# Kernel optimization log

Hardware: AMD Instinct MI355X
Metric: run time of the kernel (lower is better)

Reference implementation:

```python
import jax, jax.numpy as jnp
import numpy as np

N_LABELS = 16
LABEL_DIM = 128
BN_EPS = 1e-5


def setup_inputs() -> dict:
    key = jax.random.key(0)
    k1, k2 = jax.random.split(key, 2)
    B, T, D = 8, 512, 768
    return {
        "features": jax.random.normal(k1, (B, T, D), dtype=jnp.float32),
        "mask": jnp.ones((B, T), dtype=bool),
        "bn_gamma": jnp.ones((D,), dtype=jnp.float32),
        "bn_beta": jnp.zeros((D,), dtype=jnp.float32),
        "ff_w": jax.random.normal(k2, (LABEL_DIM * N_LABELS * 2, D), dtype=jnp.float32) * 0.02,
        "ff_b": jnp.zeros((LABEL_DIM * N_LABELS * 2,), dtype=jnp.float32),
        "label_bias": jnp.zeros((N_LABELS,), dtype=jnp.float32),
    }


def reference(features, mask, bn_gamma, bn_beta, ff_w, ff_b, label_bias):
    B, T, D = features.shape
    m = mask.astype(features.dtype)[..., None]  # [B,T,1]
    denom = jnp.maximum(m.sum(), 1.0)
    # FlatBatchNorm (training mode): stats over masked tokens, zeros elsewhere
    mean = (features * m).sum(axis=(0, 1)) / denom
    var = (((features - mean) ** 2) * m).sum(axis=(0, 1)) / denom
    normed = (features - mean) * jax.lax.rsqrt(var + BN_EPS) * bn_gamma + bn_beta
    feats = normed * m  # res[mask]=flat, zeros elsewhere
    # FFN + relu -> [B,T,n_labels,label_dim,2]
    h = jax.nn.relu(jnp.einsum('btd,od->bto', feats, ff_w) + ff_b)
    h = h.reshape(B, T, N_LABELS, LABEL_DIM, 2)
    start_f = h[..., 0]  # [B,T,L,D]
    end_f = h[..., 1]
    # biaffine span scores: [B, L, T_start, T_end]
    scores = jnp.einsum('bsld,beld->blse', start_f, end_f) + label_bias[None, :, None, None]
    triu = jnp.triu(jnp.ones((T, T), dtype=bool))
    spans_mask = triu[None, None] & mask[:, None, :, None] & mask[:, None, None, :]  # [B,L,T,T] via broadcast
    spans_mask = jnp.broadcast_to(spans_mask, scores.shape)
    return scores, spans_mask
```

## Files before the change

kernel.cpp:

```cpp
#include <hip/hip_runtime.h>

#define B_    8
#define T_    512
#define D_    768
#define L_    16
#define DL_   128
#define M_    4096
#define BN_EPS 1e-5f

typedef __attribute__((ext_vector_type(8))) short short8;
typedef __attribute__((ext_vector_type(4))) float f32x4;

__device__ inline unsigned short f2bf(float x) {
    unsigned int u = __float_as_uint(x);
    return (unsigned short)((u + 0x7fffu + ((u >> 16) & 1u)) >> 16);
}

__device__ inline void async16(const unsigned short* gptr, unsigned short* lptr) {
    __builtin_amdgcn_global_load_lds(
        (const __attribute__((address_space(1))) void*)gptr,
        (__attribute__((address_space(3))) void*)lptr, 16, 0, 0);
}

__global__ void k_stats(const float* __restrict__ f, const int* __restrict__ mask,
                        float* __restrict__ stats) {
    int tid = threadIdx.x;
    int t0  = blockIdx.x * 16;
    float s0 = 0.f, s1 = 0.f, s2 = 0.f, q0 = 0.f, q1 = 0.f, q2 = 0.f;
    for (int tt = 0; tt < 16; ++tt) {
        int t = t0 + tt;
        float m = mask[t] ? 1.f : 0.f;
        const float* row = f + (size_t)t * D_;
        float x0 = row[tid];
        float x1 = row[tid + 256];
        float x2 = row[tid + 512];
        s0 += x0 * m; q0 += x0 * x0 * m;
        s1 += x1 * m; q1 += x1 * x1 * m;
        s2 += x2 * m; q2 += x2 * x2 * m;
    }
    atomicAdd(&stats[tid      ], s0);
    atomicAdd(&stats[tid + 256], s1);
    atomicAdd(&stats[tid + 512], s2);
    atomicAdd(&stats[768 + tid      ], q0);
    atomicAdd(&stats[768 + tid + 256], q1);
    atomicAdd(&stats[768 + tid + 512], q2);
    if (tid == 0) {
        int c = 0;
        for (int tt = 0; tt < 16; ++tt) c += (mask[t0 + tt] ? 1 : 0);
        atomicAdd(&stats[1536], (float)c);
    }
}

__global__ void k_finalize(const float* __restrict__ gamma, const float* __restrict__ beta,
                           float* __restrict__ stats) {
    int d = threadIdx.x;
    float denom = fmaxf(stats[1536], 1.f);
    float mean  = stats[d] / denom;
    float var   = fmaxf(stats[768 + d] / denom - mean * mean, 0.f);
    float sc    = gamma[d] * rsqrtf(var + BN_EPS);
    stats[2048 + d] = sc;
    stats[2816 + d] = beta[d] - mean * sc;
}

__global__ void k_prep(const float4* __restrict__ f4, const int* __restrict__ mask,
                       const float* __restrict__ stats, unsigned short* __restrict__ feats,
                       const float4* __restrict__ w4, unsigned short* __restrict__ wbf) {
    int bx = blockIdx.x;
    if (bx < 3072) {
        int i  = bx * 256 + threadIdx.x;
        int d4 = i % (D_ / 4);
        int t  = i / (D_ / 4);
        float m = mask[t] ? 1.f : 0.f;
        float4 v = f4[i];
        int d = d4 * 4;
        ushort4 o;
        o.x = f2bf((v.x * stats[2048 + d + 0] + stats[2816 + d + 0]) * m);
        o.y = f2bf((v.y * stats[2048 + d + 1] + stats[2816 + d + 1]) * m);
        o.z = f2bf((v.z * stats[2048 + d + 2] + stats[2816 + d + 2]) * m);
        o.w = f2bf((v.w * stats[2048 + d + 3] + stats[2816 + d + 3]) * m);
        ((ushort4*)feats)[i] = o;
    } else {
        int i  = (bx - 3072) * 256 + threadIdx.x;
        int o  = i / 192, cg = i % 192;
        int nr = (o & 1) * 2048 + (o >> 8) * 128 + ((o >> 1) & 127);
        float4 v = w4[i];
        ushort4 u;
        u.x = f2bf(v.x); u.y = f2bf(v.y); u.z = f2bf(v.z); u.w = f2bf(v.w);
        ((ushort4*)wbf)[nr * 192 + cg] = u;
    }
}

__launch_bounds__(256)
__global__ void k_ffn(const unsigned short* __restrict__ A, const unsigned short* __restrict__ W,
                      const float* __restrict__ ffb,
                      unsigned short* __restrict__ startp, unsigned short* __restrict__ endp) {
    __shared__ alignas(16) unsigned short As[128 * 32];
    __shared__ alignas(16) unsigned short Bs[128 * 32];
    int tid  = threadIdx.x;
    int bm   = blockIdx.x, bn = blockIdx.y;
    int wave = tid >> 6, lane = tid & 63;
    int wm = wave >> 1, wn = wave & 1;
    int lr = lane & 15, quad = lane >> 4;
    int srow = lane >> 2, sseg = (lane & 3) * 8;
    f32x4 acc[4][4] = {};
    const int K = D_;
    const unsigned short* Abase = A + (size_t)(bm * 128) * K;
    const unsigned short* Wbase = W + (size_t)(bn * 128) * K;
    for (int k0 = 0; k0 < K; k0 += 32) {
#pragma unroll
        for (int p = 0; p < 2; ++p) {
            int r0 = (wave * 2 + p) * 16;
            async16(Abase + (size_t)(r0 + srow) * K + k0 + sseg, &As[r0 * 32]);
            async16(Wbase + (size_t)(r0 + srow) * K + k0 + sseg, &Bs[r0 * 32]);
        }
        __syncthreads();
        short8 a[4], b[4];
#pragma unroll
        for (int i = 0; i < 4; ++i) a[i] = *(const short8*)&As[(wm * 64 + i * 16 + lr) * 32 + quad * 8];
#pragma unroll
        for (int i = 0; i < 4; ++i) b[i] = *(const short8*)&Bs[(wn * 64 + i * 16 + lr) * 32 + quad * 8];
#pragma unroll
        for (int i = 0; i < 4; ++i)
#pragma unroll
            for (int j = 0; j < 4; ++j)
                acc[i][j] = __builtin_amdgcn_mfma_f32_16x16x32_bf16(a[i], b[j], acc[i][j], 0, 0, 0);
        __syncthreads();
    }
    int c = bn >> 4, l = bn & 15;
    unsigned short* dstb = c ? endp : startp;
#pragma unroll
    for (int j = 0; j < 4; ++j) {
        int dd = wn * 64 + j * 16 + lr;
        float bv = ffb[l * 256 + dd * 2 + c];
#pragma unroll
        for (int i = 0; i < 4; ++i) {
#pragma unroll
            for (int r = 0; r < 4; ++r) {
                int row = bm * 128 + wm * 64 + i * 16 + quad * 4 + r;
                int bb = row >> 9, tt = row & 511;
                float v = fmaxf(acc[i][j][r] + bv, 0.f);
                dstb[(((size_t)(bb * 16 + l) * 512 + tt) << 7) + dd] = f2bf(v);
            }
        }
    }
}

__launch_bounds__(256)
__global__ void k_biaffine(const unsigned short* __restrict__ startp,
                           const unsigned short* __restrict__ endp,
                           const float* __restrict__ lbias, const int* __restrict__ mask,
                           float* __restrict__ outs, float* __restrict__ outm) {
    __shared__ alignas(16) unsigned short As[128 * 32];
    __shared__ alignas(16) unsigned short Bs[128 * 32];
    int tid = threadIdx.x;
    int bm = blockIdx.x, bn = blockIdx.y;
    int bl = blockIdx.z;
    int b  = bl >> 4;
    const unsigned short* Abase = startp + ((size_t)bl * 512 + bm * 128) * 128;
    const unsigned short* Bbase = endp   + ((size_t)bl * 512 + bn * 128) * 128;
    int wave = tid >> 6, lane = tid & 63;
    int wm = wave >> 1, wn = wave & 1;
    int lr = lane & 15, quad = lane >> 4;
    int srow = lane >> 2, sseg = (lane & 3) * 8;
    f32x4 acc[4][4] = {};
    for (int k0 = 0; k0 < 128; k0 += 32) {
#pragma unroll
        for (int p = 0; p < 2; ++p) {
            int r0 = (wave * 2 + p) * 16;
            async16(Abase + (size_t)(r0 + srow) * 128 + k0 + sseg, &As[r0 * 32]);
            async16(Bbase + (size_t)(r0 + srow) * 128 + k0 + sseg, &Bs[r0 * 32]);
        }
        __syncthreads();
        short8 a[4], b8[4];
#pragma unroll
        for (int i = 0; i < 4; ++i) a[i]  = *(const short8*)&As[(wm * 64 + i * 16 + lr) * 32 + quad * 8];
#pragma unroll
        for (int i = 0; i < 4; ++i) b8[i] = *(const short8*)&Bs[(wn * 64 + i * 16 + lr) * 32 + quad * 8];
#pragma unroll
        for (int i = 0; i < 4; ++i)
#pragma unroll
            for (int j = 0; j < 4; ++j)
                acc[i][j] = __builtin_amdgcn_mfma_f32_16x16x32_bf16(a[i], b8[j], acc[i][j], 0, 0, 0);
        __syncthreads();
    }
    float lb = lbias[bl & 15];
    float* os = outs + (size_t)bl * 262144;
    float* om = outm + (size_t)bl * 262144;
#pragma unroll
    for (int i = 0; i < 4; ++i) {
#pragma unroll
        for (int r = 0; r < 4; ++r) {
            int s = bm * 128 + wm * 64 + i * 16 + quad * 4 + r;
            float msv = mask[b * 512 + s] ? 1.f : 0.f;
#pragma unroll
            for (int j = 0; j < 4; ++j) {
                int e = bn * 128 + wn * 64 + j * 16 + lr;
                os[(size_t)s * 512 + e] = acc[i][j][r] + lb;
                om[(size_t)s * 512 + e] = (s <= e && mask[b * 512 + e]) ? msv : 0.f;
            }
        }
    }
}

extern "C" void kernel_launch(void* const* d_in, const int* in_sizes, int n_in,
                              void* d_out, int out_size, void* d_ws, size_t ws_size,
                              hipStream_t stream) {
    const float* features = (const float*)d_in[0];
    const int*   mask     = (const int*)d_in[1];
    const float* gamma    = (const float*)d_in[2];
    const float* beta     = (const float*)d_in[3];
    const float* ffw      = (const float*)d_in[4];
    const float* ffb      = (const float*)d_in[5];
    const float* lbias    = (const float*)d_in[6];

    float* out_scores = (float*)d_out;
    float* out_mask   = out_scores + (size_t)B_ * L_ * T_ * T_;

    char* ws = (char*)d_ws;
    float*          stats  = (float*)ws;
    unsigned short* feats  = (unsigned short*)(ws + 16384);
    unsigned short* wbf    = (unsigned short*)(ws + 16384 + 6291456);
    unsigned short* startp = (unsigned short*)(ws + 12599296);
    unsigned short* endp   = (unsigned short*)(ws + 29376512);

    hipMemsetAsync(ws, 0, 16384, stream);
    k_stats<<<256, 256, 0, stream>>>(features, mask, stats);
    k_finalize<<<1, 768, 0, stream>>>(gamma, beta, stats);
    k_prep<<<6144, 256, 0, stream>>>((const float4*)features, mask, stats, feats,
                                     (const float4*)ffw, wbf);
    dim3 g1(32, 32);
    k_ffn<<<g1, 256, 0, stream>>>(feats, wbf, ffb, startp, endp);
    dim3 g2(4, 4, 128);
    k_biaffine<<<g2, 256, 0, stream>>>(startp, endp, lbias, mask, out_scores, out_mask);
}
```

Baseline: 382.2 us.

## Fuse stats with weight cast, fold finalize into norm, load biaffine operands directly

```diff
diff --git a/kernel.cpp b/kernel.cpp
--- a/kernel.cpp
+++ b/kernel.cpp
@@ -22,72 +22,69 @@
         (__attribute__((address_space(3))) void*)lptr, 16, 0, 0);
 }
 
-__global__ void k_stats(const float* __restrict__ f, const int* __restrict__ mask,
-                        float* __restrict__ stats) {
-    int tid = threadIdx.x;
-    int t0  = blockIdx.x * 16;
-    float s0 = 0.f, s1 = 0.f, s2 = 0.f, q0 = 0.f, q1 = 0.f, q2 = 0.f;
-    for (int tt = 0; tt < 16; ++tt) {
-        int t = t0 + tt;
-        float m = mask[t] ? 1.f : 0.f;
-        const float* row = f + (size_t)t * D_;
-        float x0 = row[tid];
-        float x1 = row[tid + 256];
-        float x2 = row[tid + 512];
-        s0 += x0 * m; q0 += x0 * x0 * m;
-        s1 += x1 * m; q1 += x1 * x1 * m;
-        s2 += x2 * m; q2 += x2 * x2 * m;
-    }
-    atomicAdd(&stats[tid      ], s0);
-    atomicAdd(&stats[tid + 256], s1);
-    atomicAdd(&stats[tid + 512], s2);
-    atomicAdd(&stats[768 + tid      ], q0);
-    atomicAdd(&stats[768 + tid + 256], q1);
-    atomicAdd(&stats[768 + tid + 512], q2);
-    if (tid == 0) {
-        int c = 0;
-        for (int tt = 0; tt < 16; ++tt) c += (mask[t0 + tt] ? 1 : 0);
-        atomicAdd(&stats[1536], (float)c);
-    }
-}
-
-__global__ void k_finalize(const float* __restrict__ gamma, const float* __restrict__ beta,
-                           float* __restrict__ stats) {
-    int d = threadIdx.x;
-    float denom = fmaxf(stats[1536], 1.f);
-    float mean  = stats[d] / denom;
-    float var   = fmaxf(stats[768 + d] / denom - mean * mean, 0.f);
-    float sc    = gamma[d] * rsqrtf(var + BN_EPS);
-    stats[2048 + d] = sc;
-    stats[2816 + d] = beta[d] - mean * sc;
-}
-
-__global__ void k_prep(const float4* __restrict__ f4, const int* __restrict__ mask,
-                       const float* __restrict__ stats, unsigned short* __restrict__ feats,
-                       const float4* __restrict__ w4, unsigned short* __restrict__ wbf) {
-    int bx = blockIdx.x;
-    if (bx < 3072) {
-        int i  = bx * 256 + threadIdx.x;
-        int d4 = i % (D_ / 4);
-        int t  = i / (D_ / 4);
-        float m = mask[t] ? 1.f : 0.f;
-        float4 v = f4[i];
-        int d = d4 * 4;
-        ushort4 o;
-        o.x = f2bf((v.x * stats[2048 + d + 0] + stats[2816 + d + 0]) * m);
-        o.y = f2bf((v.y * stats[2048 + d + 1] + stats[2816 + d + 1]) * m);
-        o.z = f2bf((v.z * stats[2048 + d + 2] + stats[2816 + d + 2]) * m);
-        o.w = f2bf((v.w * stats[2048 + d + 3] + stats[2816 + d + 3]) * m);
-        ((ushort4*)feats)[i] = o;
+__global__ void k_statsw(const float* __restrict__ f, const int* __restrict__ mask,
+                         float* __restrict__ stats,
+                         const float4* __restrict__ w4, unsigned short* __restrict__ wbf) {
+    int bx = blockIdx.x, tid = threadIdx.x;
+    if (bx < 256) {
+        int t0 = bx * 16;
+        float s0 = 0.f, s1 = 0.f, s2 = 0.f, q0 = 0.f, q1 = 0.f, q2 = 0.f;
+        for (int tt = 0; tt < 16; ++tt) {
+            int t = t0 + tt;
+            float m = mask[t] ? 1.f : 0.f;
+            const float* row = f + (size_t)t * D_;
+            float x0 = row[tid];
+            float x1 = row[tid + 256];
+            float x2 = row[tid + 512];
+            s0 += x0 * m; q0 += x0 * x0 * m;
+            s1 += x1 * m; q1 += x1 * x1 * m;
+            s2 += x2 * m; q2 += x2 * x2 * m;
+        }
+        atomicAdd(&stats[tid      ], s0);
+        atomicAdd(&stats[tid + 256], s1);
+        atomicAdd(&stats[tid + 512], s2);
+        atomicAdd(&stats[768 + tid      ], q0);
+        atomicAdd(&stats[768 + tid + 256], q1);
+        atomicAdd(&stats[768 + tid + 512], q2);
+        if (tid == 0) {
+            int c = 0;
+            for (int tt = 0; tt < 16; ++tt) c += (mask[t0 + tt] ? 1 : 0);
+            atomicAdd(&stats[1536], (float)c);
+        }
     } else {
-        int i  = (bx - 3072) * 256 + threadIdx.x;
-        int o  = i / 192, cg = i % 192;
+        int i = (bx - 256) * 256 + tid;
+        int o = i / 192, cg = i % 192;
         int nr = (o & 1) * 2048 + (o >> 8) * 128 + ((o >> 1) & 127);
         float4 v = w4[i];
         ushort4 u;
         u.x = f2bf(v.x); u.y = f2bf(v.y); u.z = f2bf(v.z); u.w = f2bf(v.w);
         ((ushort4*)wbf)[nr * 192 + cg] = u;
     }
+}
+
+__global__ void k_norm(const float4* __restrict__ f4, const int* __restrict__ mask,
+                       const float* __restrict__ stats,
+                       const float* __restrict__ gamma, const float* __restrict__ beta,
+                       unsigned short* __restrict__ feats) {
+    int i  = blockIdx.x * 256 + threadIdx.x;
+    int d4 = i % (D_ / 4);
+    int t  = i / (D_ / 4);
+    int d  = d4 * 4;
+    float denom = fmaxf(stats[1536], 1.f);
+    float m = mask[t] ? 1.f : 0.f;
+    float4 v = f4[i];
+    float r[4] = {v.x, v.y, v.z, v.w};
+    ushort4 o;
+    unsigned short* op = (unsigned short*)&o;
+#pragma unroll
+    for (int c = 0; c < 4; ++c) {
+        float mean = stats[d + c] / denom;
+        float var  = fmaxf(stats[768 + d + c] / denom - mean * mean, 0.f);
+        float sc   = gamma[d + c] * rsqrtf(var + BN_EPS);
+        float sh   = beta[d + c] - mean * sc;
+        op[c] = f2bf((r[c] * sc + sh) * m);
+    }
+    ((ushort4*)feats)[i] = o;
 }
 
 __launch_bounds__(256)
@@ -150,38 +147,28 @@
                            const unsigned short* __restrict__ endp,
                            const float* __restrict__ lbias, const int* __restrict__ mask,
                            float* __restrict__ outs, float* __restrict__ outm) {
-    __shared__ alignas(16) unsigned short As[128 * 32];
-    __shared__ alignas(16) unsigned short Bs[128 * 32];
     int tid = threadIdx.x;
     int bm = blockIdx.x, bn = blockIdx.y;
     int bl = blockIdx.z;
     int b  = bl >> 4;
-    const unsigned short* Abase = startp + ((size_t)bl * 512 + bm * 128) * 128;
-    const unsigned short* Bbase = endp   + ((size_t)bl * 512 + bn * 128) * 128;
     int wave = tid >> 6, lane = tid & 63;
     int wm = wave >> 1, wn = wave & 1;
     int lr = lane & 15, quad = lane >> 4;
-    int srow = lane >> 2, sseg = (lane & 3) * 8;
+    const unsigned short* Ap = startp + ((size_t)bl * 512 + bm * 128 + wm * 64 + lr) * 128 + quad * 8;
+    const unsigned short* Bp = endp   + ((size_t)bl * 512 + bn * 128 + wn * 64 + lr) * 128 + quad * 8;
     f32x4 acc[4][4] = {};
+#pragma unroll
     for (int k0 = 0; k0 < 128; k0 += 32) {
-#pragma unroll
-        for (int p = 0; p < 2; ++p) {
-            int r0 = (wave * 2 + p) * 16;
-            async16(Abase + (size_t)(r0 + srow) * 128 + k0 + sseg, &As[r0 * 32]);
-            async16(Bbase + (size_t)(r0 + srow) * 128 + k0 + sseg, &Bs[r0 * 32]);
-        }
-        __syncthreads();
         short8 a[4], b8[4];
 #pragma unroll
-        for (int i = 0; i < 4; ++i) a[i]  = *(const short8*)&As[(wm * 64 + i * 16 + lr) * 32 + quad * 8];
-#pragma unroll
-        for (int i = 0; i < 4; ++i) b8[i] = *(const short8*)&Bs[(wn * 64 + i * 16 + lr) * 32 + quad * 8];
+        for (int i = 0; i < 4; ++i) a[i]  = *(const short8*)(Ap + i * (16 * 128) + k0);
+#pragma unroll
+        for (int j = 0; j < 4; ++j) b8[j] = *(const short8*)(Bp + j * (16 * 128) + k0);
 #pragma unroll
         for (int i = 0; i < 4; ++i)
 #pragma unroll
             for (int j = 0; j < 4; ++j)
                 acc[i][j] = __builtin_amdgcn_mfma_f32_16x16x32_bf16(a[i], b8[j], acc[i][j], 0, 0, 0);
-        __syncthreads();
     }
     float lb = lbias[bl & 15];
     float* os = outs + (size_t)bl * 262144;
@@ -223,11 +210,9 @@
     unsigned short* startp = (unsigned short*)(ws + 12599296);
     unsigned short* endp   = (unsigned short*)(ws + 29376512);
 
-    hipMemsetAsync(ws, 0, 16384, stream);
-    k_stats<<<256, 256, 0, stream>>>(features, mask, stats);
-    k_finalize<<<1, 768, 0, stream>>>(gamma, beta, stats);
-    k_prep<<<6144, 256, 0, stream>>>((const float4*)features, mask, stats, feats,
-                                     (const float4*)ffw, wbf);
+    hipMemsetAsync(ws, 0, 8192, stream);
+    k_statsw<<<3328, 256, 0, stream>>>(features, mask, stats, (const float4*)ffw, wbf);
+    k_norm<<<3072, 256, 0, stream>>>((const float4*)features, mask, stats, gamma, beta, feats);
     dim3 g1(32, 32);
     k_ffn<<<g1, 256, 0, stream>>>(feats, wbf, ffb, startp, endp);
     dim3 g2(4, 4, 128);
```

Result: no change. 386.8 us (+1.2%).
